# Optimization experiments

Measured on AMD Instinct MI355X. Metric: run time of the kernel, lower is better.

The kernel has to match this reference:

```python
import jax, jax.numpy as jnp
import numpy as np

N = 8192
F_IN = 256
F_OUT = 64
ALPHA = 0.2  # LeakyReLU negative slope
MASK_VAL = -9e15


def setup_inputs() -> dict:
    key = jax.random.key(0)
    k1, k2, k3, k4 = jax.random.split(key, 4)
    h = jax.random.normal(k1, (N, F_IN), dtype=jnp.float32)
    adj = jax.random.randint(k2, (N, N), 0, 2, dtype=jnp.int32)  # 0/1 dense adjacency
    # Parameters (original creates them inside forward with xavier init; here fixed inputs)
    W = jax.random.normal(k3, (F_IN, F_OUT), dtype=jnp.float32) * (1.414 * np.sqrt(2.0 / (F_IN + F_OUT)))
    a = jax.random.normal(k4, (2 * F_OUT, 1), dtype=jnp.float32) * (1.414 * np.sqrt(2.0 / (2 * F_OUT + 1)))
    return {"h": h, "adj": adj, "W": W, "a": a}


def reference(h, adj, W, a):
    # Wh: [N, F_OUT]
    Wh = h @ W
    # e_ij = LeakyReLU(a^T [Wh_i ; Wh_j]) computed via broadcast instead of the
    f_src = Wh @ a[:F_OUT, 0]   # [N] contribution of row node i
    f_dst = Wh @ a[F_OUT:, 0]   # [N] contribution of col node j
    e = jax.nn.leaky_relu(f_src[:, None] + f_dst[None, :], negative_slope=ALPHA)  # [N, N]
    # adj-masked row softmax
    scores = jnp.where(adj > 0, e, MASK_VAL)
    attention = jax.nn.softmax(scores, axis=1)
    # dropout omitted (deterministic eval reference)
    h_prime = attention @ Wh  # [N, F_OUT]
    return jax.nn.elu(h_prime)  # concat=True branch
```

## Files before the change

kernel.cpp:

```cpp
#include <hip/hip_runtime.h>
#include <hip/hip_bf16.h>

#define NN 8192
#define FIN 256
#define FOUT 64
#define L2E 1.4426950408889634f
#define PADK 40

typedef __attribute__((ext_vector_type(8))) short short8;
typedef __attribute__((ext_vector_type(4))) float f32x4;
typedef __attribute__((ext_vector_type(4))) int   iv4;

#define BAR() do { \
  __asm__ __volatile__("s_waitcnt lgkmcnt(0)" ::: "memory"); \
  __builtin_amdgcn_s_barrier(); \
  __asm__ __volatile__("" ::: "memory"); \
} while (0)

__device__ __forceinline__ unsigned short f2bf(float x){
  unsigned u = __float_as_uint(x);
  u += 0x7FFFu + ((u >> 16) & 1u);
  return (unsigned short)(u >> 16);
}

__device__ __forceinline__ unsigned spread4(unsigned x){
  x &= 0xFFu;
  x = (x | (x << 12)) & 0x000F000Fu;
  x = (x | (x << 6))  & 0x03030303u;
  x = (x | (x << 3))  & 0x11111111u;
  return x;
}

__device__ __forceinline__ void cv_process(iv4 d, int l,
                                           unsigned* __restrict__ mp, int g){
  unsigned n = (unsigned)(d.x != 0)        | ((unsigned)(d.y != 0) << 1)
             | ((unsigned)(d.z != 0) << 2) | ((unsigned)(d.w != 0) << 3);
  unsigned long long B0 = __ballot((n & 1u) != 0);
  unsigned long long B1 = __ballot((n & 2u) != 0);
  unsigned long long B2 = __ballot((n & 4u) != 0);
  unsigned long long B3 = __ballot((n & 8u) != 0);
  const int hi = l & 4, sh = (l & 3) * 8;
  unsigned b0 = (unsigned)((hi ? (B0 >> 32) : B0) >> sh);
  unsigned b1 = (unsigned)((hi ? (B1 >> 32) : B1) >> sh);
  unsigned b2 = (unsigned)((hi ? (B2 >> 32) : B2) >> sh);
  unsigned b3 = (unsigned)((hi ? (B3 >> 32) : B3) >> sh);
  unsigned word = spread4(b0) | (spread4(b1) << 1)
                | (spread4(b2) << 2) | (spread4(b3) << 3);
  if (l < 8) mp[g*8 + l] = word;
}

__global__ __launch_bounds__(256) void k_pm(const float* __restrict__ h,
    const float* __restrict__ W, const float* __restrict__ a,
    const int* __restrict__ adj, unsigned short* __restrict__ WhT,
    float* __restrict__ fs, float* __restrict__ fd,
    unsigned* __restrict__ gmax_u, unsigned* __restrict__ mask){
  const int bid = blockIdx.x, t = threadIdx.x;
  const int l = t & 63, wv = t >> 6;
  if (bid % 3 == 0){
    const int pid = bid / 3;
    __shared__ float Ws[128*64];
    __shared__ float hs[8][128];
    const int rb = pid * 8;
    float acc0 = 0.f, acc1 = 0.f;
    for (int half = 0; half < 2; ++half){
      if (half) __syncthreads();
      for (int i = t; i < 2048; i += 256)
        ((float4*)Ws)[i] = ((const float4*)W)[half*2048 + i];
      {
        int rr = t >> 5, cc = t & 31;
        ((float4*)&hs[rr][0])[cc] =
            *(const float4*)(h + (size_t)(rb+rr)*FIN + half*128 + cc*4);
      }
      __syncthreads();
      #pragma unroll 8
      for (int k = 0; k < 128; ++k){
        float wval = Ws[k*64 + l];
        acc0 = fmaf(hs[wv*2+0][k], wval, acc0);
        acc1 = fmaf(hs[wv*2+1][k], wval, acc1);
      }
    }
    const int r0 = rb + wv*2, r1 = r0 + 1;
    float a1 = a[l], a2 = a[64 + l];
    float p0 = acc0*a1, q0 = acc0*a2, p1 = acc1*a1, q1 = acc1*a2;
    #pragma unroll
    for (int m = 1; m < 64; m <<= 1){
      p0 += __shfl_xor(p0, m); q0 += __shfl_xor(q0, m);
      p1 += __shfl_xor(p1, m); q1 += __shfl_xor(q1, m);
    }
    if (l == 0){
      fs[r0] = p0*L2E; fs[r1] = p1*L2E; fd[r0] = q0*L2E; fd[r1] = q1*L2E;
      atomicMax(gmax_u, __float_as_uint(q0*L2E + 64.0f));
      atomicMax(gmax_u, __float_as_uint(q1*L2E + 64.0f));
    }
    WhT[(size_t)l*NN + r0] = f2bf(acc0);
    WhT[(size_t)l*NN + r1] = f2bf(acc1);
  } else {
    const int cid = bid - bid/3 - 1;
    const unsigned rowid = (unsigned)cid*4u + (unsigned)wv;
    const iv4* __restrict__ ap = (const iv4*)(adj + (size_t)rowid*8192u) + l;
    unsigned* __restrict__ mp = mask + rowid*256u;
    iv4 d0 = ap[0*64], d1 = ap[1*64], d2 = ap[2*64], d3 = ap[3*64];
    iv4 d4 = ap[4*64], d5 = ap[5*64], d6 = ap[6*64], d7 = ap[7*64];
    #pragma unroll 1
    for (int i = 0; i < 32; i += 8){
      cv_process(d0, l, mp, i+0); if (i+ 8 < 32) d0 = ap[(i+ 8)*64];
      cv_process(d1, l, mp, i+1); if (i+ 9 < 32) d1 = ap[(i+ 9)*64];
      cv_process(d2, l, mp, i+2); if (i+10 < 32) d2 = ap[(i+10)*64];
      cv_process(d3, l, mp, i+3); if (i+11 < 32) d3 = ap[(i+11)*64];
      cv_process(d4, l, mp, i+4); if (i+12 < 32) d4 = ap[(i+12)*64];
      cv_process(d5, l, mp, i+5); if (i+13 < 32) d5 = ap[(i+13)*64];
      cv_process(d6, l, mp, i+6); if (i+14 < 32) d6 = ap[(i+14)*64];
      cv_process(d7, l, mp, i+7); if (i+15 < 32) d7 = ap[(i+15)*64];
    }
  }
}

__device__ __forceinline__ void attn_math(unsigned mbits, f32x4 fv0, f32x4 fv1,
    short8 w0, short8 w1, short8 w2, short8 w3,
    float fsrL, float mL, f32x4* acc, float& s0, float& s1){
  const float fv[8] = {fv0[0],fv0[1],fv0[2],fv0[3], fv1[0],fv1[1],fv1[2],fv1[3]};
  float w[8];
  #pragma unroll
  for (int j = 0; j < 8; ++j){
    float x  = fsrL + fv[j];
    float tt = fmaxf(x, 0.2f*x);
    float e  = __builtin_amdgcn_exp2f(tt - mL);
    w[j] = (mbits & (1u << j)) ? e : 0.0f;
  }
  s0 += (w[0]+w[2]) + (w[4]+w[6]);
  s1 += (w[1]+w[3]) + (w[5]+w[7]);
  short8 af;
  __hip_bfloat162* afp = (__hip_bfloat162*)&af;
  #pragma unroll
  for (int j = 0; j < 4; ++j)
    afp[j] = __float22bfloat162_rn(make_float2(w[2*j], w[2*j+1]));
  acc[0] = __builtin_amdgcn_mfma_f32_16x16x32_bf16(af, w0, acc[0], 0,0,0);
  acc[1] = __builtin_amdgcn_mfma_f32_16x16x32_bf16(af, w1, acc[1], 0,0,0);
  acc[2] = __builtin_amdgcn_mfma_f32_16x16x32_bf16(af, w2, acc[2], 0,0,0);
  acc[3] = __builtin_amdgcn_mfma_f32_16x16x32_bf16(af, w3, acc[3], 0,0,0);
}

__global__ __launch_bounds__(256, 4) void k_attn(const unsigned* __restrict__ mask,
    const unsigned short* __restrict__ WhT, const float* __restrict__ fs,
    const float* __restrict__ fd, const unsigned* __restrict__ gmax_u,
    float* __restrict__ acc_out, float* __restrict__ s_out){
  __shared__ unsigned short bslab[2][64*PADK];
  __shared__ float fslab[2][32];
  const int t = threadIdx.x, l = t & 63, wv = t >> 6;
  const int g = blockIdx.x & 127;
  const int kchunk = blockIdx.x >> 7;
  const int row = l & 15, quad = l >> 4;
  const int ibase = g*64 + wv*16;
  const int irow  = ibase + row;
  const float gmaxL = __uint_as_float(*gmax_u) - 64.0f;
  const float fsrL  = fs[irow];
  const float xL    = fsrL + gmaxL;
  const float mL    = fmaxf(xL, 0.2f*xL);

  const unsigned jbase = (unsigned)kchunk*1024u;
  const unsigned m_off = (unsigned)irow*256u + (jbase >> 5);
  const unsigned sg_off = (unsigned)l*8192u + jbase + (unsigned)wv*8u;
  const int      sl_off = l*PADK + wv*8;
  const int      qsh    = quad*8;

  f32x4 acc[4];
  #pragma unroll
  for (int nb = 0; nb < 4; ++nb) acc[nb] = (f32x4){0.f,0.f,0.f,0.f};

  {
    short8 v = *(const short8*)(WhT + sg_off);
    *(short8*)&bslab[0][sl_off] = v;
    if (t < 32) fslab[0][t] = fd[jbase + t];
  }
  unsigned m0 = mask[m_off + 0] >> qsh;
  unsigned m1 = mask[m_off + 1] >> qsh;

  float s0 = 0.f, s1 = 0.f;
  short8 nw; float nf = 0.f;

  #pragma unroll 1
  for (int s = 0; s < 32; s += 2){
    BAR();
    nw = *(const short8*)(WhT + sg_off + (s+1)*32);
    if (t < 32) nf = fd[jbase + (s+1)*32 + t];
    {
      f32x4 fv0 = *(const f32x4*)&fslab[0][qsh];
      f32x4 fv1 = *(const f32x4*)&fslab[0][qsh + 4];
      short8 w0 = *(const short8*)&bslab[0][( 0 + row)*PADK + qsh];
      short8 w1 = *(const short8*)&bslab[0][(16 + row)*PADK + qsh];
      short8 w2 = *(const short8*)&bslab[0][(32 + row)*PADK + qsh];
      short8 w3 = *(const short8*)&bslab[0][(48 + row)*PADK + qsh];
      attn_math(m0, fv0, fv1, w0, w1, w2, w3, fsrL, mL, acc, s0, s1);
    }
    if (s + 2 < 32) m0 = mask[m_off + s + 2] >> qsh;
    *(short8*)&bslab[1][sl_off] = nw;
    if (t < 32) fslab[1][t] = nf;

    BAR();
    if (s + 2 < 32){
      nw = *(const short8*)(WhT + sg_off + (s+2)*32);
      if (t < 32) nf = fd[jbase + (s+2)*32 + t];
    }
    {
      f32x4 fv0 = *(const f32x4*)&fslab[1][qsh];
      f32x4 fv1 = *(const f32x4*)&fslab[1][qsh + 4];
      short8 w0 = *(const short8*)&bslab[1][( 0 + row)*PADK + qsh];
      short8 w1 = *(const short8*)&bslab[1][(16 + row)*PADK + qsh];
      short8 w2 = *(const short8*)&bslab[1][(32 + row)*PADK + qsh];
      short8 w3 = *(const short8*)&bslab[1][(48 + row)*PADK + qsh];
      attn_math(m1, fv0, fv1, w0, w1, w2, w3, fsrL, mL, acc, s0, s1);
    }
    if (s + 3 < 32) m1 = mask[m_off + s + 3] >> qsh;
    if (s + 2 < 32){
      *(short8*)&bslab[0][sl_off] = nw;
      if (t < 32) fslab[0][t] = nf;
    }
  }

  float sacc = s0 + s1;
  sacc += __shfl_xor(sacc, 16);
  sacc += __shfl_xor(sacc, 32);
  if (l < 16) s_out[kchunk*NN + ibase + l] = sacc;
  float* op = acc_out + ((size_t)kchunk*NN + ibase)*FOUT;
  #pragma unroll
  for (int nb = 0; nb < 4; ++nb)
    #pragma unroll
    for (int r = 0; r < 4; ++r)
      op[(quad*4 + r)*FOUT + nb*16 + row] = acc[nb][r];
}

__global__ __launch_bounds__(256) void k_out(const float* __restrict__ acc,
    const float* __restrict__ s, float* __restrict__ out){
  const int idx = blockIdx.x*256 + threadIdx.x;
  const int i = idx >> 6;
  float num = 0.f, den = 0.f;
  #pragma unroll
  for (int ks = 0; ks < 8; ++ks){
    num += acc[idx + (size_t)ks*(NN*FOUT)];
    den += s[i + ks*NN];
  }
  float x = num / den;
  out[idx] = (x > 0.f) ? x : (__expf(x) - 1.0f);
}

extern "C" void kernel_launch(void* const* d_in, const int* in_sizes, int n_in,
                              void* d_out, int out_size, void* d_ws, size_t ws_size,
                              hipStream_t stream){
  const float* h   = (const float*)d_in[0];
  const int*   adj = (const int*)d_in[1];
  const float* W   = (const float*)d_in[2];
  const float* a   = (const float*)d_in[3];
  char* ws = (char*)d_ws;
  unsigned short* WhT = (unsigned short*)ws;
  float*    fs     = (float*)(ws + (1u<<20));
  float*    fd     = (float*)(ws + (1u<<20) + 32768);
  unsigned* gmax_u = (unsigned*)(ws + (1u<<20) + 65536);
  float*    acc    = (float*)(ws + (2u<<20));
  float*    s_ws   = (float*)(ws + (20u<<20));
  unsigned* mask   = (unsigned*)(ws + (48u<<20));

  (void)hipMemsetAsync(gmax_u, 0, 4, stream);
  k_pm<<<3072, 256, 0, stream>>>(h, W, a, adj, WhT, fs, fd, gmax_u, mask);
  k_attn<<<1024, 256, 0, stream>>>(mask, WhT, fs, fd, gmax_u, acc, s_ws);
  k_out<<<2048, 256, 0, stream>>>(acc, s_ws, (float*)d_out);
}
```

Measured before the change: 444.6 us.

## Read int adjacency directly in attention kernel instead of building a bitmask

Removes the separate pass that packed the 256 MB int32 adjacency into a bitmask and the bitmask round-trip through workspace. The attention kernel now loads two int4 vectors of adjacency per lane per step and tests them directly. The adjacency is still read once from HBM, but now inside the attention loop, which raises per-iteration memory traffic and register use there and may hurt latency hiding. The projection kernel becomes a plain 1024-block launch.

```diff
diff --git a/kernel.cpp b/kernel.cpp
--- a/kernel.cpp
+++ b/kernel.cpp
@@ -23,109 +23,62 @@
   return (unsigned short)(u >> 16);
 }
 
-__device__ __forceinline__ unsigned spread4(unsigned x){
-  x &= 0xFFu;
-  x = (x | (x << 12)) & 0x000F000Fu;
-  x = (x | (x << 6))  & 0x03030303u;
-  x = (x | (x << 3))  & 0x11111111u;
-  return x;
-}
-
-__device__ __forceinline__ void cv_process(iv4 d, int l,
-                                           unsigned* __restrict__ mp, int g){
-  unsigned n = (unsigned)(d.x != 0)        | ((unsigned)(d.y != 0) << 1)
-             | ((unsigned)(d.z != 0) << 2) | ((unsigned)(d.w != 0) << 3);
-  unsigned long long B0 = __ballot((n & 1u) != 0);
-  unsigned long long B1 = __ballot((n & 2u) != 0);
-  unsigned long long B2 = __ballot((n & 4u) != 0);
-  unsigned long long B3 = __ballot((n & 8u) != 0);
-  const int hi = l & 4, sh = (l & 3) * 8;
-  unsigned b0 = (unsigned)((hi ? (B0 >> 32) : B0) >> sh);
-  unsigned b1 = (unsigned)((hi ? (B1 >> 32) : B1) >> sh);
-  unsigned b2 = (unsigned)((hi ? (B2 >> 32) : B2) >> sh);
-  unsigned b3 = (unsigned)((hi ? (B3 >> 32) : B3) >> sh);
-  unsigned word = spread4(b0) | (spread4(b1) << 1)
-                | (spread4(b2) << 2) | (spread4(b3) << 3);
-  if (l < 8) mp[g*8 + l] = word;
-}
-
 __global__ __launch_bounds__(256) void k_pm(const float* __restrict__ h,
     const float* __restrict__ W, const float* __restrict__ a,
-    const int* __restrict__ adj, unsigned short* __restrict__ WhT,
-    float* __restrict__ fs, float* __restrict__ fd,
-    unsigned* __restrict__ gmax_u, unsigned* __restrict__ mask){
-  const int bid = blockIdx.x, t = threadIdx.x;
+    unsigned short* __restrict__ WhT, float* __restrict__ fs,
+    float* __restrict__ fd, unsigned* __restrict__ gmax_u){
+  const int t = threadIdx.x;
   const int l = t & 63, wv = t >> 6;
-  if (bid % 3 == 0){
-    const int pid = bid / 3;
-    __shared__ float Ws[128*64];
-    __shared__ float hs[8][128];
-    const int rb = pid * 8;
-    float acc0 = 0.f, acc1 = 0.f;
-    for (int half = 0; half < 2; ++half){
-      if (half) __syncthreads();
-      for (int i = t; i < 2048; i += 256)
-        ((float4*)Ws)[i] = ((const float4*)W)[half*2048 + i];
-      {
-        int rr = t >> 5, cc = t & 31;
-        ((float4*)&hs[rr][0])[cc] =
-            *(const float4*)(h + (size_t)(rb+rr)*FIN + half*128 + cc*4);
-      }
-      __syncthreads();
-      #pragma unroll 8
-      for (int k = 0; k < 128; ++k){
-        float wval = Ws[k*64 + l];
-        acc0 = fmaf(hs[wv*2+0][k], wval, acc0);
-        acc1 = fmaf(hs[wv*2+1][k], wval, acc1);
-      }
-    }
-    const int r0 = rb + wv*2, r1 = r0 + 1;
-    float a1 = a[l], a2 = a[64 + l];
-    float p0 = acc0*a1, q0 = acc0*a2, p1 = acc1*a1, q1 = acc1*a2;
-    #pragma unroll
-    for (int m = 1; m < 64; m <<= 1){
-      p0 += __shfl_xor(p0, m); q0 += __shfl_xor(q0, m);
-      p1 += __shfl_xor(p1, m); q1 += __shfl_xor(q1, m);
-    }
-    if (l == 0){
-      fs[r0] = p0*L2E; fs[r1] = p1*L2E; fd[r0] = q0*L2E; fd[r1] = q1*L2E;
-      atomicMax(gmax_u, __float_as_uint(q0*L2E + 64.0f));
-      atomicMax(gmax_u, __float_as_uint(q1*L2E + 64.0f));
-    }
-    WhT[(size_t)l*NN + r0] = f2bf(acc0);
-    WhT[(size_t)l*NN + r1] = f2bf(acc1);
-  } else {
-    const int cid = bid - bid/3 - 1;
-    const unsigned rowid = (unsigned)cid*4u + (unsigned)wv;
-    const iv4* __restrict__ ap = (const iv4*)(adj + (size_t)rowid*8192u) + l;
-    unsigned* __restrict__ mp = mask + rowid*256u;
-    iv4 d0 = ap[0*64], d1 = ap[1*64], d2 = ap[2*64], d3 = ap[3*64];
-    iv4 d4 = ap[4*64], d5 = ap[5*64], d6 = ap[6*64], d7 = ap[7*64];
-    #pragma unroll 1
-    for (int i = 0; i < 32; i += 8){
-      cv_process(d0, l, mp, i+0); if (i+ 8 < 32) d0 = ap[(i+ 8)*64];
-      cv_process(d1, l, mp, i+1); if (i+ 9 < 32) d1 = ap[(i+ 9)*64];
-      cv_process(d2, l, mp, i+2); if (i+10 < 32) d2 = ap[(i+10)*64];
-      cv_process(d3, l, mp, i+3); if (i+11 < 32) d3 = ap[(i+11)*64];
-      cv_process(d4, l, mp, i+4); if (i+12 < 32) d4 = ap[(i+12)*64];
-      cv_process(d5, l, mp, i+5); if (i+13 < 32) d5 = ap[(i+13)*64];
-      cv_process(d6, l, mp, i+6); if (i+14 < 32) d6 = ap[(i+14)*64];
-      cv_process(d7, l, mp, i+7); if (i+15 < 32) d7 = ap[(i+15)*64];
-    }
-  }
-}
-
-__device__ __forceinline__ void attn_math(unsigned mbits, f32x4 fv0, f32x4 fv1,
+  __shared__ float Ws[128*64];
+  __shared__ float hs[8][128];
+  const int rb = blockIdx.x * 8;
+  float acc0 = 0.f, acc1 = 0.f;
+  for (int half = 0; half < 2; ++half){
+    if (half) __syncthreads();
+    for (int i = t; i < 2048; i += 256)
+      ((float4*)Ws)[i] = ((const float4*)W)[half*2048 + i];
+    {
+      int rr = t >> 5, cc = t & 31;
+      ((float4*)&hs[rr][0])[cc] =
+          *(const float4*)(h + (size_t)(rb+rr)*FIN + half*128 + cc*4);
+    }
+    __syncthreads();
+    #pragma unroll 8
+    for (int k = 0; k < 128; ++k){
+      float wval = Ws[k*64 + l];
+      acc0 = fmaf(hs[wv*2+0][k], wval, acc0);
+      acc1 = fmaf(hs[wv*2+1][k], wval, acc1);
+    }
+  }
+  const int r0 = rb + wv*2, r1 = r0 + 1;
+  float a1 = a[l], a2 = a[64 + l];
+  float p0 = acc0*a1, q0 = acc0*a2, p1 = acc1*a1, q1 = acc1*a2;
+  #pragma unroll
+  for (int m = 1; m < 64; m <<= 1){
+    p0 += __shfl_xor(p0, m); q0 += __shfl_xor(q0, m);
+    p1 += __shfl_xor(p1, m); q1 += __shfl_xor(q1, m);
+  }
+  if (l == 0){
+    fs[r0] = p0*L2E; fs[r1] = p1*L2E; fd[r0] = q0*L2E; fd[r1] = q1*L2E;
+    atomicMax(gmax_u, __float_as_uint(q0*L2E + 64.0f));
+    atomicMax(gmax_u, __float_as_uint(q1*L2E + 64.0f));
+  }
+  WhT[(size_t)l*NN + r0] = f2bf(acc0);
+  WhT[(size_t)l*NN + r1] = f2bf(acc1);
+}
+
+__device__ __forceinline__ void attn_math(iv4 da, iv4 db, f32x4 fv0, f32x4 fv1,
     short8 w0, short8 w1, short8 w2, short8 w3,
     float fsrL, float mL, f32x4* acc, float& s0, float& s1){
   const float fv[8] = {fv0[0],fv0[1],fv0[2],fv0[3], fv1[0],fv1[1],fv1[2],fv1[3]};
+  const int   dv[8] = {da.x,da.y,da.z,da.w, db.x,db.y,db.z,db.w};
   float w[8];
   #pragma unroll
   for (int j = 0; j < 8; ++j){
     float x  = fsrL + fv[j];
     float tt = fmaxf(x, 0.2f*x);
     float e  = __builtin_amdgcn_exp2f(tt - mL);
-    w[j] = (mbits & (1u << j)) ? e : 0.0f;
+    w[j] = dv[j] ? e : 0.0f;
   }
   s0 += (w[0]+w[2]) + (w[4]+w[6]);
   s1 += (w[1]+w[3]) + (w[5]+w[7]);
@@ -140,7 +93,7 @@
   acc[3] = __builtin_amdgcn_mfma_f32_16x16x32_bf16(af, w3, acc[3], 0,0,0);
 }
 
-__global__ __launch_bounds__(256, 4) void k_attn(const unsigned* __restrict__ mask,
+__global__ __launch_bounds__(256, 4) void k_attn(const int* __restrict__ adj,
     const unsigned short* __restrict__ WhT, const float* __restrict__ fs,
     const float* __restrict__ fd, const unsigned* __restrict__ gmax_u,
     float* __restrict__ acc_out, float* __restrict__ s_out){
@@ -158,10 +111,12 @@
   const float mL    = fmaxf(xL, 0.2f*xL);
 
   const unsigned jbase = (unsigned)kchunk*1024u;
-  const unsigned m_off = (unsigned)irow*256u + (jbase >> 5);
   const unsigned sg_off = (unsigned)l*8192u + jbase + (unsigned)wv*8u;
   const int      sl_off = l*PADK + wv*8;
   const int      qsh    = quad*8;
+
+  const iv4* __restrict__ ap =
+      (const iv4*)(adj + (size_t)irow*8192u + jbase + (unsigned)qsh);
 
   f32x4 acc[4];
   #pragma unroll
@@ -172,8 +127,8 @@
     *(short8*)&bslab[0][sl_off] = v;
     if (t < 32) fslab[0][t] = fd[jbase + t];
   }
-  unsigned m0 = mask[m_off + 0] >> qsh;
-  unsigned m1 = mask[m_off + 1] >> qsh;
+  iv4 c0a = ap[0], c0b = ap[1];
+  iv4 c1a = ap[8], c1b = ap[9];
 
   float s0 = 0.f, s1 = 0.f;
   short8 nw; float nf = 0.f;
@@ -190,9 +145,9 @@
       short8 w1 = *(const short8*)&bslab[0][(16 + row)*PADK + qsh];
       short8 w2 = *(const short8*)&bslab[0][(32 + row)*PADK + qsh];
       short8 w3 = *(const short8*)&bslab[0][(48 + row)*PADK + qsh];
-      attn_math(m0, fv0, fv1, w0, w1, w2, w3, fsrL, mL, acc, s0, s1);
-    }
-    if (s + 2 < 32) m0 = mask[m_off + s + 2] >> qsh;
+      attn_math(c0a, c0b, fv0, fv1, w0, w1, w2, w3, fsrL, mL, acc, s0, s1);
+    }
+    if (s + 2 < 32){ c0a = ap[(s+2)*8]; c0b = ap[(s+2)*8 + 1]; }
     *(short8*)&bslab[1][sl_off] = nw;
     if (t < 32) fslab[1][t] = nf;
 
@@ -208,9 +163,9 @@
       short8 w1 = *(const short8*)&bslab[1][(16 + row)*PADK + qsh];
       short8 w2 = *(const short8*)&bslab[1][(32 + row)*PADK + qsh];
       short8 w3 = *(const short8*)&bslab[1][(48 + row)*PADK + qsh];
-      attn_math(m1, fv0, fv1, w0, w1, w2, w3, fsrL, mL, acc, s0, s1);
-    }
-    if (s + 3 < 32) m1 = mask[m_off + s + 3] >> qsh;
+      attn_math(c1a, c1b, fv0, fv1, w0, w1, w2, w3, fsrL, mL, acc, s0, s1);
+    }
+    if (s + 3 < 32){ c1a = ap[(s+3)*8]; c1b = ap[(s+3)*8 + 1]; }
     if (s + 2 < 32){
       *(short8*)&bslab[0][sl_off] = nw;
       if (t < 32) fslab[0][t] = nf;
@@ -257,10 +212,9 @@
   unsigned* gmax_u = (unsigned*)(ws + (1u<<20) + 65536);
   float*    acc    = (float*)(ws + (2u<<20));
   float*    s_ws   = (float*)(ws + (20u<<20));
-  unsigned* mask   = (unsigned*)(ws + (48u<<20));
 
   (void)hipMemsetAsync(gmax_u, 0, 4, stream);
-  k_pm<<<3072, 256, 0, stream>>>(h, W, a, adj, WhT, fs, fd, gmax_u, mask);
-  k_attn<<<1024, 256, 0, stream>>>(mask, WhT, fs, fd, gmax_u, acc, s_ws);
+  k_pm<<<1024, 256, 0, stream>>>(h, W, a, WhT, fs, fd, gmax_u);
+  k_attn<<<1024, 256, 0, stream>>>(adj, WhT, fs, fd, gmax_u, acc, s_ws);
   k_out<<<2048, 256, 0, stream>>>(acc, s_ws, (float*)d_out);
 }
```

After: 516.9 us. 16.3% more time.

## Load WhT and fd fragments straight from global into registers, drop LDS staging

Applied to the files above, without the earlier changes.

The attention kernel no longer stages WhT and fd tiles through double-buffered shared memory with barriers. Each lane now loads its own MFMA B-operand fragments and fd values straight from global memory, prefetched two steps ahead in registers. This removes LDS traffic and block-wide synchronisation. In exchange it adds more global or cache requests, since the four waves each reload the same data instead of sharing one cooperative load, and it raises register pressure from the prefetch buffers.

```diff
diff --git a/kernel.cpp b/kernel.cpp
--- a/kernel.cpp
+++ b/kernel.cpp
@@ -5,17 +5,10 @@
 #define FIN 256
 #define FOUT 64
 #define L2E 1.4426950408889634f
-#define PADK 40
 
 typedef __attribute__((ext_vector_type(8))) short short8;
 typedef __attribute__((ext_vector_type(4))) float f32x4;
 typedef __attribute__((ext_vector_type(4))) int   iv4;
-
-#define BAR() do { \
-  __asm__ __volatile__("s_waitcnt lgkmcnt(0)" ::: "memory"); \
-  __builtin_amdgcn_s_barrier(); \
-  __asm__ __volatile__("" ::: "memory"); \
-} while (0)
 
 __device__ __forceinline__ unsigned short f2bf(float x){
   unsigned u = __float_as_uint(x);
@@ -144,8 +137,6 @@
     const unsigned short* __restrict__ WhT, const float* __restrict__ fs,
     const float* __restrict__ fd, const unsigned* __restrict__ gmax_u,
     float* __restrict__ acc_out, float* __restrict__ s_out){
-  __shared__ unsigned short bslab[2][64*PADK];
-  __shared__ float fslab[2][32];
   const int t = threadIdx.x, l = t & 63, wv = t >> 6;
   const int g = blockIdx.x & 127;
   const int kchunk = blockIdx.x >> 7;
@@ -159,62 +150,55 @@
 
   const unsigned jbase = (unsigned)kchunk*1024u;
   const unsigned m_off = (unsigned)irow*256u + (jbase >> 5);
-  const unsigned sg_off = (unsigned)l*8192u + jbase + (unsigned)wv*8u;
-  const int      sl_off = l*PADK + wv*8;
-  const int      qsh    = quad*8;
+  const int      qsh   = quad*8;
+
+  const unsigned short* __restrict__ wp0 = WhT + (size_t)( 0+row)*NN + jbase + qsh;
+  const unsigned short* __restrict__ wp1 = WhT + (size_t)(16+row)*NN + jbase + qsh;
+  const unsigned short* __restrict__ wp2 = WhT + (size_t)(32+row)*NN + jbase + qsh;
+  const unsigned short* __restrict__ wp3 = WhT + (size_t)(48+row)*NN + jbase + qsh;
+  const float* __restrict__ fp = fd + jbase + qsh;
 
   f32x4 acc[4];
   #pragma unroll
   for (int nb = 0; nb < 4; ++nb) acc[nb] = (f32x4){0.f,0.f,0.f,0.f};
 
-  {
-    short8 v = *(const short8*)(WhT + sg_off);
-    *(short8*)&bslab[0][sl_off] = v;
-    if (t < 32) fslab[0][t] = fd[jbase + t];
-  }
-  unsigned m0 = mask[m_off + 0] >> qsh;
-  unsigned m1 = mask[m_off + 1] >> qsh;
+  short8 c0 = *(const short8*)(wp0);
+  short8 c1 = *(const short8*)(wp1);
+  short8 c2 = *(const short8*)(wp2);
+  short8 c3 = *(const short8*)(wp3);
+  short8 n0 = *(const short8*)(wp0 + 32);
+  short8 n1 = *(const short8*)(wp1 + 32);
+  short8 n2 = *(const short8*)(wp2 + 32);
+  short8 n3 = *(const short8*)(wp3 + 32);
+  f32x4 fva = *(const f32x4*)(fp);
+  f32x4 fvb = *(const f32x4*)(fp + 4);
+  unsigned mc = mask[m_off + 0] >> qsh;
+  unsigned mn = mask[m_off + 1] >> qsh;
 
   float s0 = 0.f, s1 = 0.f;
-  short8 nw; float nf = 0.f;
 
   #pragma unroll 1
-  for (int s = 0; s < 32; s += 2){
-    BAR();
-    nw = *(const short8*)(WhT + sg_off + (s+1)*32);
-    if (t < 32) nf = fd[jbase + (s+1)*32 + t];
-    {
-      f32x4 fv0 = *(const f32x4*)&fslab[0][qsh];
-      f32x4 fv1 = *(const f32x4*)&fslab[0][qsh + 4];
-      short8 w0 = *(const short8*)&bslab[0][( 0 + row)*PADK + qsh];
-      short8 w1 = *(const short8*)&bslab[0][(16 + row)*PADK + qsh];
-      short8 w2 = *(const short8*)&bslab[0][(32 + row)*PADK + qsh];
-      short8 w3 = *(const short8*)&bslab[0][(48 + row)*PADK + qsh];
-      attn_math(m0, fv0, fv1, w0, w1, w2, w3, fsrL, mL, acc, s0, s1);
-    }
-    if (s + 2 < 32) m0 = mask[m_off + s + 2] >> qsh;
-    *(short8*)&bslab[1][sl_off] = nw;
-    if (t < 32) fslab[1][t] = nf;
-
-    BAR();
+  for (int s = 0; s < 32; ++s){
+    short8 p0 = n0, p1 = n1, p2 = n2, p3 = n3;
+    unsigned pm = mn;
     if (s + 2 < 32){
-      nw = *(const short8*)(WhT + sg_off + (s+2)*32);
-      if (t < 32) nf = fd[jbase + (s+2)*32 + t];
-    }
-    {
-      f32x4 fv0 = *(const f32x4*)&fslab[1][qsh];
-      f32x4 fv1 = *(const f32x4*)&fslab[1][qsh + 4];
-      short8 w0 = *(const short8*)&bslab[1][( 0 + row)*PADK + qsh];
-      short8 w1 = *(const short8*)&bslab[1][(16 + row)*PADK + qsh];
-      short8 w2 = *(const short8*)&bslab[1][(32 + row)*PADK + qsh];
-      short8 w3 = *(const short8*)&bslab[1][(48 + row)*PADK + qsh];
-      attn_math(m1, fv0, fv1, w0, w1, w2, w3, fsrL, mL, acc, s0, s1);
-    }
-    if (s + 3 < 32) m1 = mask[m_off + s + 3] >> qsh;
-    if (s + 2 < 32){
-      *(short8*)&bslab[0][sl_off] = nw;
-      if (t < 32) fslab[0][t] = nf;
-    }
+      const int o = (s+2)*32;
+      p0 = *(const short8*)(wp0 + o);
+      p1 = *(const short8*)(wp1 + o);
+      p2 = *(const short8*)(wp2 + o);
+      p3 = *(const short8*)(wp3 + o);
+      pm = mask[m_off + s + 2] >> qsh;
+    }
+    f32x4 pva = fva, pvb = fvb;
+    if (s + 1 < 32){
+      pva = *(const f32x4*)(fp + (s+1)*32);
+      pvb = *(const f32x4*)(fp + (s+1)*32 + 4);
+    }
+    attn_math(mc, fva, fvb, c0, c1, c2, c3, fsrL, mL, acc, s0, s1);
+    c0 = n0; c1 = n1; c2 = n2; c3 = n3;
+    n0 = p0; n1 = p1; n2 = p2; n3 = p3;
+    fva = pva; fvb = pvb;
+    mc = mn; mn = pm;
   }
 
   float sacc = s0 + s1;
```

Result: slower. 492.4 us (+10.8%).

## Stage 128-column slabs per barrier in attention and vectorize output kernel

Applied to the files above, without the earlier changes.

The attention kernel now stages 128 columns of WhT and fd per shared-memory buffer instead of 32, and loads the mask as uint4 so that four mask words arrive per load. Each barrier-separated phase now runs four MFMA sub-steps, which cuts barrier and loop overhead by a factor of four. In exchange it uses more LDS and registers, which could lower occupancy. The output kernel is changed to process float4 per thread, with a reciprocal multiply in place of a division and a quarter as many blocks.

```diff
diff --git a/kernel.cpp b/kernel.cpp
--- a/kernel.cpp
+++ b/kernel.cpp
@@ -5,7 +5,7 @@
 #define FIN 256
 #define FOUT 64
 #define L2E 1.4426950408889634f
-#define PADK 40
+#define PADK3 136
 
 typedef __attribute__((ext_vector_type(8))) short short8;
 typedef __attribute__((ext_vector_type(4))) float f32x4;
@@ -140,12 +140,25 @@
   acc[3] = __builtin_amdgcn_mfma_f32_16x16x32_bf16(af, w3, acc[3], 0,0,0);
 }
 
+__device__ __forceinline__ void attn_sub(const unsigned short* __restrict__ bs,
+    const float* __restrict__ fsl, int sub, int row, int qsh, unsigned mword,
+    float fsrL, float mL, f32x4* acc, float& s0, float& s1){
+  const int o = sub*32 + qsh;
+  f32x4 fv0 = *(const f32x4*)&fsl[o];
+  f32x4 fv1 = *(const f32x4*)&fsl[o + 4];
+  short8 w0 = *(const short8*)&bs[( 0 + row)*PADK3 + o];
+  short8 w1 = *(const short8*)&bs[(16 + row)*PADK3 + o];
+  short8 w2 = *(const short8*)&bs[(32 + row)*PADK3 + o];
+  short8 w3 = *(const short8*)&bs[(48 + row)*PADK3 + o];
+  attn_math(mword >> qsh, fv0, fv1, w0, w1, w2, w3, fsrL, mL, acc, s0, s1);
+}
+
 __global__ __launch_bounds__(256, 4) void k_attn(const unsigned* __restrict__ mask,
     const unsigned short* __restrict__ WhT, const float* __restrict__ fs,
     const float* __restrict__ fd, const unsigned* __restrict__ gmax_u,
     float* __restrict__ acc_out, float* __restrict__ s_out){
-  __shared__ unsigned short bslab[2][64*PADK];
-  __shared__ float fslab[2][32];
+  __shared__ unsigned short bslab[2][64*PADK3];
+  __shared__ float fslab[2][128];
   const int t = threadIdx.x, l = t & 63, wv = t >> 6;
   const int g = blockIdx.x & 127;
   const int kchunk = blockIdx.x >> 7;
@@ -158,9 +171,10 @@
   const float mL    = fmaxf(xL, 0.2f*xL);
 
   const unsigned jbase = (unsigned)kchunk*1024u;
-  const unsigned m_off = (unsigned)irow*256u + (jbase >> 5);
-  const unsigned sg_off = (unsigned)l*8192u + jbase + (unsigned)wv*8u;
-  const int      sl_off = l*PADK + wv*8;
+  const uint4* __restrict__ mq =
+      (const uint4*)(mask + (size_t)irow*256u + (jbase >> 5));
+  const unsigned sg_off = (unsigned)l*8192u + jbase + (unsigned)wv*32u;
+  const int      sl_off = l*PADK3 + wv*32;
   const int      qsh    = quad*8;
 
   f32x4 acc[4];
@@ -168,52 +182,61 @@
   for (int nb = 0; nb < 4; ++nb) acc[nb] = (f32x4){0.f,0.f,0.f,0.f};
 
   {
-    short8 v = *(const short8*)(WhT + sg_off);
-    *(short8*)&bslab[0][sl_off] = v;
-    if (t < 32) fslab[0][t] = fd[jbase + t];
-  }
-  unsigned m0 = mask[m_off + 0] >> qsh;
-  unsigned m1 = mask[m_off + 1] >> qsh;
+    const unsigned short* p = WhT + sg_off;
+    *(short8*)&bslab[0][sl_off]      = *(const short8*)(p);
+    *(short8*)&bslab[0][sl_off + 8]  = *(const short8*)(p + 8);
+    *(short8*)&bslab[0][sl_off + 16] = *(const short8*)(p + 16);
+    *(short8*)&bslab[0][sl_off + 24] = *(const short8*)(p + 24);
+    if (t < 128) fslab[0][t] = fd[jbase + t];
+  }
+  uint4 M0 = mq[0];
+  uint4 M1 = mq[1];
 
   float s0 = 0.f, s1 = 0.f;
-  short8 nw; float nf = 0.f;
+  short8 nw0, nw1, nw2, nw3; float nf = 0.f;
 
   #pragma unroll 1
-  for (int s = 0; s < 32; s += 2){
+  for (int s = 0; s < 8; s += 2){
     BAR();
-    nw = *(const short8*)(WhT + sg_off + (s+1)*32);
-    if (t < 32) nf = fd[jbase + (s+1)*32 + t];
     {
-      f32x4 fv0 = *(const f32x4*)&fslab[0][qsh];
-      f32x4 fv1 = *(const f32x4*)&fslab[0][qsh + 4];
-      short8 w0 = *(const short8*)&bslab[0][( 0 + row)*PADK + qsh];
-      short8 w1 = *(const short8*)&bslab[0][(16 + row)*PADK + qsh];
-      short8 w2 = *(const short8*)&bslab[0][(32 + row)*PADK + qsh];
-      short8 w3 = *(const short8*)&bslab[0][(48 + row)*PADK + qsh];
-      attn_math(m0, fv0, fv1, w0, w1, w2, w3, fsrL, mL, acc, s0, s1);
-    }
-    if (s + 2 < 32) m0 = mask[m_off + s + 2] >> qsh;
-    *(short8*)&bslab[1][sl_off] = nw;
-    if (t < 32) fslab[1][t] = nf;
+      const unsigned short* p = WhT + sg_off + (s+1)*128;
+      nw0 = *(const short8*)(p);
+      nw1 = *(const short8*)(p + 8);
+      nw2 = *(const short8*)(p + 16);
+      nw3 = *(const short8*)(p + 24);
+    }
+    if (t < 128) nf = fd[jbase + (s+1)*128 + t];
+    attn_sub(bslab[0], fslab[0], 0, row, qsh, M0.x, fsrL, mL, acc, s0, s1);
+    attn_sub(bslab[0], fslab[0], 1, row, qsh, M0.y, fsrL, mL, acc, s0, s1);
+    attn_sub(bslab[0], fslab[0], 2, row, qsh, M0.z, fsrL, mL, acc, s0, s1);
+    attn_sub(bslab[0], fslab[0], 3, row, qsh, M0.w, fsrL, mL, acc, s0, s1);
+    if (s + 2 < 8) M0 = mq[s + 2];
+    *(short8*)&bslab[1][sl_off]      = nw0;
+    *(short8*)&bslab[1][sl_off + 8]  = nw1;
+    *(short8*)&bslab[1][sl_off + 16] = nw2;
+    *(short8*)&bslab[1][sl_off + 24] = nw3;
+    if (t < 128) fslab[1][t] = nf;
 
     BAR();
-    if (s + 2 < 32){
-      nw = *(const short8*)(WhT + sg_off + (s+2)*32);
-      if (t < 32) nf = fd[jbase + (s+2)*32 + t];
-    }
-    {
-      f32x4 fv0 = *(const f32x4*)&fslab[1][qsh];
-      f32x4 fv1 = *(const f32x4*)&fslab[1][qsh + 4];
-      short8 w0 = *(const short8*)&bslab[1][( 0 + row)*PADK + qsh];
-      short8 w1 = *(const short8*)&bslab[1][(16 + row)*PADK + qsh];
-      short8 w2 = *(const short8*)&bslab[1][(32 + row)*PADK + qsh];
-      short8 w3 = *(const short8*)&bslab[1][(48 + row)*PADK + qsh];
-      attn_math(m1, fv0, fv1, w0, w1, w2, w3, fsrL, mL, acc, s0, s1);
-    }
-    if (s + 3 < 32) m1 = mask[m_off + s + 3] >> qsh;
-    if (s + 2 < 32){
-      *(short8*)&bslab[0][sl_off] = nw;
-      if (t < 32) fslab[0][t] = nf;
+    if (s + 2 < 8){
+      const unsigned short* p = WhT + sg_off + (s+2)*128;
+      nw0 = *(const short8*)(p);
+      nw1 = *(const short8*)(p + 8);
+      nw2 = *(const short8*)(p + 16);
+      nw3 = *(const short8*)(p + 24);
+      nf = (t < 128) ? fd[jbase + (s+2)*128 + t] : 0.f;
+    }
+    attn_sub(bslab[1], fslab[1], 0, row, qsh, M1.x, fsrL, mL, acc, s0, s1);
+    attn_sub(bslab[1], fslab[1], 1, row, qsh, M1.y, fsrL, mL, acc, s0, s1);
+    attn_sub(bslab[1], fslab[1], 2, row, qsh, M1.z, fsrL, mL, acc, s0, s1);
+    attn_sub(bslab[1], fslab[1], 3, row, qsh, M1.w, fsrL, mL, acc, s0, s1);
+    if (s + 3 < 8) M1 = mq[s + 3];
+    if (s + 2 < 8){
+      *(short8*)&bslab[0][sl_off]      = nw0;
+      *(short8*)&bslab[0][sl_off + 8]  = nw1;
+      *(short8*)&bslab[0][sl_off + 16] = nw2;
+      *(short8*)&bslab[0][sl_off + 24] = nw3;
+      if (t < 128) fslab[0][t] = nf;
     }
   }
 
@@ -231,16 +254,24 @@
 
 __global__ __launch_bounds__(256) void k_out(const float* __restrict__ acc,
     const float* __restrict__ s, float* __restrict__ out){
-  const int idx = blockIdx.x*256 + threadIdx.x;
-  const int i = idx >> 6;
-  float num = 0.f, den = 0.f;
+  const int idx4 = blockIdx.x*256 + threadIdx.x;
+  const int i = idx4 >> 4;
+  float4 num = make_float4(0.f,0.f,0.f,0.f);
+  float den = 0.f;
   #pragma unroll
   for (int ks = 0; ks < 8; ++ks){
-    num += acc[idx + (size_t)ks*(NN*FOUT)];
+    float4 v = ((const float4*)acc)[idx4 + ks*(NN*FOUT/4)];
+    num.x += v.x; num.y += v.y; num.z += v.z; num.w += v.w;
     den += s[i + ks*NN];
   }
-  float x = num / den;
-  out[idx] = (x > 0.f) ? x : (__expf(x) - 1.0f);
+  const float rd = 1.0f / den;
+  float4 o;
+  float x;
+  x = num.x*rd; o.x = (x > 0.f) ? x : (__expf(x) - 1.0f);
+  x = num.y*rd; o.y = (x > 0.f) ? x : (__expf(x) - 1.0f);
+  x = num.z*rd; o.z = (x > 0.f) ? x : (__expf(x) - 1.0f);
+  x = num.w*rd; o.w = (x > 0.f) ? x : (__expf(x) - 1.0f);
+  ((float4*)out)[idx4] = o;
 }
 
 extern "C" void kernel_launch(void* const* d_in, const int* in_sizes, int n_in,
@@ -262,5 +293,5 @@
   (void)hipMemsetAsync(gmax_u, 0, 4, stream);
   k_pm<<<3072, 256, 0, stream>>>(h, W, a, adj, WhT, fs, fd, gmax_u, mask);
   k_attn<<<1024, 256, 0, stream>>>(mask, WhT, fs, fd, gmax_u, acc, s_ws);
-  k_out<<<2048, 256, 0, stream>>>(acc, s_ws, (float*)d_out);
-}
+  k_out<<<512, 256, 0, stream>>>(acc, s_ws, (float*)d_out);
+}
```

Result: slower. 504.0 us (+13.4%).
